# Kernel tuning notes

Measured on AMD Instinct MI355X. Metric: run time of the kernel, lower is better.

## Reference

```python
import jax, jax.numpy as jnp
import numpy as np

N_MBED = 384
HEAD_SIZE = 64

def setup_inputs() -> dict:
    key = jax.random.key(0)
    kx, kq, kk, kv = jax.random.split(key, 4)
    B, T = 128, 256
    x = jax.random.normal(kx, (B, T, N_MBED), dtype=jnp.float32)
    # torch nn.Linear(n_mbed, head_size, bias=False): y = x @ W^T, W:[head_size, n_mbed].
    # We store the transposed weight [n_mbed, head_size] so y = x @ W.
    s = 1.0 / np.sqrt(N_MBED)
    Wq = jax.random.uniform(kq, (N_MBED, HEAD_SIZE), jnp.float32, -s, s)
    Wk = jax.random.uniform(kk, (N_MBED, HEAD_SIZE), jnp.float32, -s, s)
    Wv = jax.random.uniform(kv, (N_MBED, HEAD_SIZE), jnp.float32, -s, s)
    return {"x": x, "Wq": Wq, "Wk": Wk, "Wv": Wv}

def reference(x, Wq, Wk, Wv):
    B, T, C = x.shape  # C = n_mbed = 384
    q = x @ Wq  # [B,T,H]
    k = x @ Wk
    v = x @ Wv
    # Faithful to source: wei = k @ q^T, scaled by C**-0.5 (C = n_mbed, not head_size)
    wei = jnp.einsum('bth,bsh->bts', k, q) * (C ** -0.5)  # [B,T,T]
    mask = jnp.tril(jnp.ones((T, T), dtype=bool))
    wei = jnp.where(mask, wei, -jnp.inf)
    wei = jax.nn.softmax(wei, axis=-1)
    # dropout omitted (eval mode / identity)
    out = jnp.einsum('bts,bsh->bth', wei, v)  # [B,T,H]
    return out
```

## Files before the change

### kernel.cpp

```cpp
#include <hip/hip_runtime.h>
#include <hip/hip_bf16.h>
#include <math.h>

constexpr int kB = 128;
constexpr int kT = 256;
constexpr int kC = 384;
constexpr int kH = 64;

using bf16x8 = __attribute__((ext_vector_type(8))) short;
using f32x4  = __attribute__((ext_vector_type(4))) float;

union BF8 { bf16x8 v; __hip_bfloat162 h[4]; };
union BF4 { short4 s; __hip_bfloat162 h[2]; };

__device__ inline bf16x8 cvt8(float4 a, float4 b) {
    BF8 u;
    u.h[0] = __float22bfloat162_rn(float2{a.x, a.y});
    u.h[1] = __float22bfloat162_rn(float2{a.z, a.w});
    u.h[2] = __float22bfloat162_rn(float2{b.x, b.y});
    u.h[3] = __float22bfloat162_rn(float2{b.z, b.w});
    return u.v;
}
__device__ inline short4 cvt4(float4 a) {
    BF4 u;
    u.h[0] = __float22bfloat162_rn(float2{a.x, a.y});
    u.h[1] = __float22bfloat162_rn(float2{a.z, a.w});
    return u.s;
}

__global__ void prep_kernel(const float* __restrict__ Wq,
                            const float* __restrict__ Wk,
                            const float* __restrict__ Wv,
                            __hip_bfloat16* __restrict__ Wt) {
    int idx = blockIdx.x * 256 + threadIdx.x;
    int n = idx / kC, c = idx % kC;
    int w = n >> 6, h = n & 63;
    const float* W = (w == 0) ? Wq : (w == 1) ? Wk : Wv;
    float val = W[c * kH + h];
    if (w == 1) val *= 0.051031036307982884f;
    Wt[idx] = __float2bfloat16(val);
}

__global__ __launch_bounds__(512, 4) void qkv_kernel(
    const float* __restrict__ x, const __hip_bfloat16* __restrict__ Wt,
    __hip_bfloat16* __restrict__ q, __hip_bfloat16* __restrict__ k,
    __hip_bfloat16* __restrict__ vT)
{
    __shared__ short As[2][64 * 72];
    __shared__ short Bs[2][192 * 72];

    const int tid  = threadIdx.x;
    const int wave = tid >> 6, lane = tid & 63;
    const int m16  = lane & 15, quad = lane >> 4;
    const int wm = wave & 1, wn = wave >> 1;
    const int m0 = blockIdx.x * 64;
    const short* wt = (const short*)Wt;

    const bool stageA = (tid < 256);
    const int am  = tid >> 2;
    const int ak0 = (tid & 3) * 16;
    const int bu  = tid - 256;

    float4 la[4]; bf16x8 lb[6];
    auto glod = [&](int k0) {
        if (stageA) {
#pragma unroll
            for (int i = 0; i < 4; ++i)
                la[i] = *(const float4*)(x + (size_t)(m0 + am) * kC + k0 + ak0 + 4 * i);
        } else {
#pragma unroll
            for (int i = 0; i < 6; ++i) {
                int c = bu + 256 * i;
                int n = c >> 3, kk = (c & 7) * 8;
                lb[i] = *(const bf16x8*)(wt + (size_t)n * kC + k0 + kk);
            }
        }
    };
    auto swr = [&](int d) {
        if (stageA) {
#pragma unroll
            for (int i = 0; i < 4; ++i)
                *(short4*)&As[d][am * 72 + ak0 + 4 * i] = cvt4(la[i]);
        } else {
#pragma unroll
            for (int i = 0; i < 6; ++i) {
                int c = bu + 256 * i;
                int n = c >> 3, kk = (c & 7) * 8;
                *(bf16x8*)&Bs[d][n * 72 + kk] = lb[i];
            }
        }
    };

    f32x4 acc[2][3];
#pragma unroll
    for (int mt = 0; mt < 2; ++mt)
#pragma unroll
        for (int j = 0; j < 3; ++j) acc[mt][j] = f32x4{0.f, 0.f, 0.f, 0.f};

    glod(0);
    swr(0);
    __syncthreads();

    for (int s = 0; s < 6; ++s) {
        const int d = s & 1;
        if (s < 5) glod((s + 1) * 64);

#pragma unroll
        for (int kf = 0; kf < 2; ++kf) {
            bf16x8 af[2], bfr[3];
#pragma unroll
            for (int mt = 0; mt < 2; ++mt)
                af[mt] = *(const bf16x8*)&As[d][(wm * 32 + mt * 16 + m16) * 72 + kf * 32 + quad * 8];
#pragma unroll
            for (int j = 0; j < 3; ++j)
                bfr[j] = *(const bf16x8*)&Bs[d][(wn * 48 + j * 16 + m16) * 72 + kf * 32 + quad * 8];
#pragma unroll
            for (int mt = 0; mt < 2; ++mt)
#pragma unroll
                for (int j = 0; j < 3; ++j)
                    acc[mt][j] = __builtin_amdgcn_mfma_f32_16x16x32_bf16(
                        af[mt], bfr[j], acc[mt][j], 0, 0, 0);
        }

        if (s < 5) swr(d ^ 1);
        __syncthreads();
    }

#pragma unroll
    for (int mt = 0; mt < 2; ++mt) {
#pragma unroll
        for (int j = 0; j < 3; ++j) {
            const int n = wn * 48 + j * 16 + m16;
            const int w = n >> 6, h = n & 63;
#pragma unroll
            for (int r = 0; r < 4; ++r) {
                const int m = m0 + wm * 32 + mt * 16 + quad * 4 + r;
                __hip_bfloat16 val = __float2bfloat16(acc[mt][j][r]);
                if (w == 0)      q[(size_t)m * kH + h] = val;
                else if (w == 1) k[(size_t)m * kH + h] = val;
                else             vT[((size_t)(m >> 8) * kH + h) * kT + (m & 255)] = val;
            }
        }
    }
}

__global__ __launch_bounds__(256) void attn_kernel(
    const __hip_bfloat16* __restrict__ qg, const __hip_bfloat16* __restrict__ kg,
    const __hip_bfloat16* __restrict__ vTg, float* __restrict__ out)
{
    __shared__ short Qs[2][64 * 72];
    __shared__ short Vs[2][64 * 72];
    __shared__ float Ps[4][16 * 68];

    const int b  = blockIdx.y;
    const int tq = blockIdx.x;
    const int tid  = threadIdx.x;
    const int wave = tid >> 6, lane = tid & 63;
    const int m16  = lane & 15, quad = lane >> 4;
    const int tband = tq * 64 + wave * 16;

    const short* qs = (const short*)qg + (size_t)b * kT * kH;
    const short* ks = (const short*)kg + (size_t)b * kT * kH;
    const short* vs = (const short*)vTg + (size_t)b * kH * kT;

    const bf16x8 ka0 = *(const bf16x8*)(ks + (size_t)(tband + m16) * kH + quad * 8);
    const bf16x8 ka1 = *(const bf16x8*)(ks + (size_t)(tband + m16) * kH + quad * 8 + 32);

    const int r0 = tid >> 3, sg = (tid & 7) * 8;

    bf16x8 lq0, lq1, lv0, lv1;
    auto glod = [&](int sc) {
        lq0 = *(const bf16x8*)(qs + (size_t)(sc + r0) * kH + sg);
        lq1 = *(const bf16x8*)(qs + (size_t)(sc + r0 + 32) * kH + sg);
        lv0 = *(const bf16x8*)(vs + (size_t)r0 * kT + sc + sg);
        lv1 = *(const bf16x8*)(vs + (size_t)(r0 + 32) * kT + sc + sg);
    };
    auto swr = [&](int d) {
        *(bf16x8*)&Qs[d][r0 * 72 + sg]        = lq0;
        *(bf16x8*)&Qs[d][(r0 + 32) * 72 + sg] = lq1;
        *(bf16x8*)&Vs[d][r0 * 72 + sg]        = lv0;
        *(bf16x8*)&Vs[d][(r0 + 32) * 72 + sg] = lv1;
    };

    f32x4 O[4];
    float m_[4], l_[4];
#pragma unroll
    for (int i = 0; i < 4; ++i) {
        O[i] = f32x4{0.f, 0.f, 0.f, 0.f};
        m_[i] = -INFINITY; l_[i] = 0.f;
    }
    float* Pw = &Ps[wave][0];

    glod(0);
    swr(0);
    __syncthreads();

    for (int i = 0; i <= tq; ++i) {
        const int d = i & 1;
        if (i < tq) glod((i + 1) * 64);

        const int jmax = (i == tq) ? wave : 3;

        f32x4 S[4];
        const f32x4 Z = f32x4{0.f, 0.f, 0.f, 0.f};
#pragma unroll
        for (int j = 0; j < 4; ++j) {
            if (j <= jmax) {
                bf16x8 qb0 = *(const bf16x8*)&Qs[d][(j * 16 + m16) * 72 + quad * 8];
                bf16x8 qb1 = *(const bf16x8*)&Qs[d][(j * 16 + m16) * 72 + 32 + quad * 8];
                S[j] = __builtin_amdgcn_mfma_f32_16x16x32_bf16(ka0, qb0, Z, 0, 0, 0);
                S[j] = __builtin_amdgcn_mfma_f32_16x16x32_bf16(ka1, qb1, S[j], 0, 0, 0);
            }
        }
        if (i == tq) {
#pragma unroll
            for (int r = 0; r < 4; ++r)
                if (m16 > quad * 4 + r) S[wave][r] = -INFINITY;
        }

        float P[4][4];
#pragma unroll
        for (int j = 0; j < 4; ++j)
#pragma unroll
            for (int r = 0; r < 4; ++r) P[j][r] = 0.f;
#pragma unroll
        for (int r = 0; r < 4; ++r) {
            float rm = -INFINITY;
#pragma unroll
            for (int j = 0; j < 4; ++j)
                if (j <= jmax) rm = fmaxf(rm, S[j][r]);
            rm = fmaxf(rm, __shfl_xor(rm, 1, 64));
            rm = fmaxf(rm, __shfl_xor(rm, 2, 64));
            rm = fmaxf(rm, __shfl_xor(rm, 4, 64));
            rm = fmaxf(rm, __shfl_xor(rm, 8, 64));
            const float mn = fmaxf(m_[r], rm);
            const float al = __expf(m_[r] - mn);
            m_[r] = mn;
            float rs = 0.f;
#pragma unroll
            for (int j = 0; j < 4; ++j) {
                if (j <= jmax) { P[j][r] = __expf(S[j][r] - mn); rs += P[j][r]; }
            }
            rs += __shfl_xor(rs, 1, 64);
            rs += __shfl_xor(rs, 2, 64);
            rs += __shfl_xor(rs, 4, 64);
            rs += __shfl_xor(rs, 8, 64);
            l_[r] = l_[r] * al + rs;
            O[0][r] *= al; O[1][r] *= al; O[2][r] *= al; O[3][r] *= al;
        }

#pragma unroll
        for (int j = 0; j < 4; ++j)
#pragma unroll
            for (int r = 0; r < 4; ++r)
                Pw[(quad * 4 + r) * 68 + j * 16 + m16] = P[j][r];
        const float* pr = Pw + m16 * 68 + quad * 8;
        bf16x8 pf0 = cvt8(*(const float4*)pr,        *(const float4*)(pr + 4));
        bf16x8 pf1 = cvt8(*(const float4*)(pr + 32), *(const float4*)(pr + 36));

#pragma unroll
        for (int ht = 0; ht < 4; ++ht) {
            bf16x8 vb0 = *(const bf16x8*)&Vs[d][(ht * 16 + m16) * 72 + quad * 8];
            bf16x8 vb1 = *(const bf16x8*)&Vs[d][(ht * 16 + m16) * 72 + 32 + quad * 8];
            O[ht] = __builtin_amdgcn_mfma_f32_16x16x32_bf16(pf0, vb0, O[ht], 0, 0, 0);
            O[ht] = __builtin_amdgcn_mfma_f32_16x16x32_bf16(pf1, vb1, O[ht], 0, 0, 0);
        }

        if (i < tq) swr(d ^ 1);
        __syncthreads();
    }

#pragma unroll
    for (int r = 0; r < 4; ++r) {
        const float inv = 1.f / l_[r];
        const size_t row = (size_t)(b * kT + tband + quad * 4 + r);
#pragma unroll
        for (int ht = 0; ht < 4; ++ht)
            out[row * kH + ht * 16 + m16] = O[ht][r] * inv;
    }
}

extern "C" void kernel_launch(void* const* d_in, const int* in_sizes, int n_in,
                              void* d_out, int out_size, void* d_ws, size_t ws_size,
                              hipStream_t stream) {
    const float* x  = (const float*)d_in[0];
    const float* Wq = (const float*)d_in[1];
    const float* Wk = (const float*)d_in[2];
    const float* Wv = (const float*)d_in[3];
    float* out = (float*)d_out;

    const size_t nqkv = (size_t)kB * kT * kH;
    __hip_bfloat16* q  = (__hip_bfloat16*)d_ws;
    __hip_bfloat16* k  = q + nqkv;
    __hip_bfloat16* vT = k + nqkv;
    __hip_bfloat16* Wt = vT + nqkv;

    prep_kernel<<<(192 * kC) / 256, 256, 0, stream>>>(Wq, Wk, Wv, Wt);
    qkv_kernel<<<(kB * kT) / 64, 512, 0, stream>>>(x, Wt, q, k, vT);
    attn_kernel<<<dim3(4, kB), 256, 0, stream>>>(q, k, vT, out);
}
```

Measured before the change: 117.4 us.

## Fuse QKV projection and causal attention into one per-batch-half kernel

Merges the QKV projection and attention kernels into one kernel. Each block handles one batch and one 128-row half of the queries, computes the needed Q/K/V^T rows directly into shared memory, then runs attention without global round-trips for q/k/vT. This removes the intermediate global traffic and a launch. In exchange the grid shrinks to 256 blocks of 512 threads, shared-memory use grows large, and the second half recomputes the projections of the first 128 rows.

```diff
diff --git a/kernel.cpp b/kernel.cpp
--- a/kernel.cpp
+++ b/kernel.cpp
@@ -26,6 +26,10 @@
     u.h[0] = __float22bfloat162_rn(float2{a.x, a.y});
     u.h[1] = __float22bfloat162_rn(float2{a.z, a.w});
     return u.s;
+}
+__device__ inline short bf1(float f) {
+    __hip_bfloat16 h = __float2bfloat16(f);
+    return *(short*)&h;
 }
 
 __global__ void prep_kernel(const float* __restrict__ Wq,
@@ -41,20 +45,28 @@
     Wt[idx] = __float2bfloat16(val);
 }
 
-__global__ __launch_bounds__(512, 4) void qkv_kernel(
+__global__ __launch_bounds__(512, 2) void fused_kernel(
     const float* __restrict__ x, const __hip_bfloat16* __restrict__ Wt,
-    __hip_bfloat16* __restrict__ q, __hip_bfloat16* __restrict__ k,
-    __hip_bfloat16* __restrict__ vT)
+    float* __restrict__ out)
 {
-    __shared__ short As[2][64 * 72];
-    __shared__ short Bs[2][192 * 72];
+    __shared__ short Qs[256 * 68];
+    __shared__ short VTs[64 * 260];
+    __shared__ short Ks[128 * 68];
+    __shared__ __attribute__((aligned(16))) char STG[73728];
+    short (*As)[64 * 72]  = (short (*)[64 * 72])STG;
+    short (*Bs)[192 * 72] = (short (*)[192 * 72])(STG + 18432);
+
+    const int b    = blockIdx.y;
+    const int half = (int)blockIdx.x ^ 1;
+    const int t0   = half * 128;
+    const int nmc  = (t0 + 128) >> 6;
 
     const int tid  = threadIdx.x;
     const int wave = tid >> 6, lane = tid & 63;
     const int m16  = lane & 15, quad = lane >> 4;
     const int wm = wave & 1, wn = wave >> 1;
-    const int m0 = blockIdx.x * 64;
     const short* wt = (const short*)Wt;
+    const float* xb = x + (size_t)b * kT * kC;
 
     const bool stageA = (tid < 256);
     const int am  = tid >> 2;
@@ -62,11 +74,11 @@
     const int bu  = tid - 256;
 
     float4 la[4]; bf16x8 lb[6];
-    auto glod = [&](int k0) {
+    auto glod = [&](int m0, int k0) {
         if (stageA) {
 #pragma unroll
             for (int i = 0; i < 4; ++i)
-                la[i] = *(const float4*)(x + (size_t)(m0 + am) * kC + k0 + ak0 + 4 * i);
+                la[i] = *(const float4*)(xb + (size_t)(m0 + am) * kC + k0 + ak0 + 4 * i);
         } else {
 #pragma unroll
             for (int i = 0; i < 6; ++i) {
@@ -91,96 +103,74 @@
         }
     };
 
-    f32x4 acc[2][3];
-#pragma unroll
-    for (int mt = 0; mt < 2; ++mt)
-#pragma unroll
-        for (int j = 0; j < 3; ++j) acc[mt][j] = f32x4{0.f, 0.f, 0.f, 0.f};
-
-    glod(0);
-    swr(0);
+    for (int mc = 0; mc < nmc; ++mc) {
+        const int m0 = mc * 64;
+
+        f32x4 acc[2][3];
+#pragma unroll
+        for (int mt = 0; mt < 2; ++mt)
+#pragma unroll
+            for (int j = 0; j < 3; ++j) acc[mt][j] = f32x4{0.f, 0.f, 0.f, 0.f};
+
+        glod(m0, 0);
+        swr(0);
+        __syncthreads();
+
+        for (int s = 0; s < 6; ++s) {
+            const int d = s & 1;
+            if (s < 5) glod(m0, (s + 1) * 64);
+#pragma unroll
+            for (int kf = 0; kf < 2; ++kf) {
+                bf16x8 af[2], bfr[3];
+#pragma unroll
+                for (int mt = 0; mt < 2; ++mt)
+                    af[mt] = *(const bf16x8*)&As[d][(wm * 32 + mt * 16 + m16) * 72 + kf * 32 + quad * 8];
+#pragma unroll
+                for (int j = 0; j < 3; ++j)
+                    bfr[j] = *(const bf16x8*)&Bs[d][(wn * 48 + j * 16 + m16) * 72 + kf * 32 + quad * 8];
+#pragma unroll
+                for (int mt = 0; mt < 2; ++mt)
+#pragma unroll
+                    for (int j = 0; j < 3; ++j)
+                        acc[mt][j] = __builtin_amdgcn_mfma_f32_16x16x32_bf16(
+                            af[mt], bfr[j], acc[mt][j], 0, 0, 0);
+            }
+            if (s < 5) swr(d ^ 1);
+            __syncthreads();
+        }
+
+#pragma unroll
+        for (int mt = 0; mt < 2; ++mt) {
+            const int mbase = m0 + wm * 32 + mt * 16 + quad * 4;
+#pragma unroll
+            for (int j = 0; j < 3; ++j) {
+                const int n = wn * 48 + j * 16 + m16;
+                const int w = n >> 6, h = n & 63;
+                if (w == 2) {
+                    float4 f = make_float4(acc[mt][j][0], acc[mt][j][1],
+                                           acc[mt][j][2], acc[mt][j][3]);
+                    *(short4*)&VTs[h * 260 + mbase] = cvt4(f);
+                } else if (w == 1) {
+                    if (m0 >= t0) {
+#pragma unroll
+                        for (int r = 0; r < 4; ++r)
+                            Ks[(mbase + r - t0) * 68 + h] = bf1(acc[mt][j][r]);
+                    }
+                } else {
+#pragma unroll
+                    for (int r = 0; r < 4; ++r)
+                        Qs[(mbase + r) * 68 + h] = bf1(acc[mt][j][r]);
+                }
+            }
+        }
+    }
     __syncthreads();
 
-    for (int s = 0; s < 6; ++s) {
-        const int d = s & 1;
-        if (s < 5) glod((s + 1) * 64);
-
-#pragma unroll
-        for (int kf = 0; kf < 2; ++kf) {
-            bf16x8 af[2], bfr[3];
-#pragma unroll
-            for (int mt = 0; mt < 2; ++mt)
-                af[mt] = *(const bf16x8*)&As[d][(wm * 32 + mt * 16 + m16) * 72 + kf * 32 + quad * 8];
-#pragma unroll
-            for (int j = 0; j < 3; ++j)
-                bfr[j] = *(const bf16x8*)&Bs[d][(wn * 48 + j * 16 + m16) * 72 + kf * 32 + quad * 8];
-#pragma unroll
-            for (int mt = 0; mt < 2; ++mt)
-#pragma unroll
-                for (int j = 0; j < 3; ++j)
-                    acc[mt][j] = __builtin_amdgcn_mfma_f32_16x16x32_bf16(
-                        af[mt], bfr[j], acc[mt][j], 0, 0, 0);
-        }
-
-        if (s < 5) swr(d ^ 1);
-        __syncthreads();
-    }
-
-#pragma unroll
-    for (int mt = 0; mt < 2; ++mt) {
-#pragma unroll
-        for (int j = 0; j < 3; ++j) {
-            const int n = wn * 48 + j * 16 + m16;
-            const int w = n >> 6, h = n & 63;
-#pragma unroll
-            for (int r = 0; r < 4; ++r) {
-                const int m = m0 + wm * 32 + mt * 16 + quad * 4 + r;
-                __hip_bfloat16 val = __float2bfloat16(acc[mt][j][r]);
-                if (w == 0)      q[(size_t)m * kH + h] = val;
-                else if (w == 1) k[(size_t)m * kH + h] = val;
-                else             vT[((size_t)(m >> 8) * kH + h) * kT + (m & 255)] = val;
-            }
-        }
-    }
-}
-
-__global__ __launch_bounds__(256) void attn_kernel(
-    const __hip_bfloat16* __restrict__ qg, const __hip_bfloat16* __restrict__ kg,
-    const __hip_bfloat16* __restrict__ vTg, float* __restrict__ out)
-{
-    __shared__ short Qs[2][64 * 72];
-    __shared__ short Vs[2][64 * 72];
-    __shared__ float Ps[4][16 * 68];
-
-    const int b  = blockIdx.y;
-    const int tq = blockIdx.x;
-    const int tid  = threadIdx.x;
-    const int wave = tid >> 6, lane = tid & 63;
-    const int m16  = lane & 15, quad = lane >> 4;
-    const int tband = tq * 64 + wave * 16;
-
-    const short* qs = (const short*)qg + (size_t)b * kT * kH;
-    const short* ks = (const short*)kg + (size_t)b * kT * kH;
-    const short* vs = (const short*)vTg + (size_t)b * kH * kT;
-
-    const bf16x8 ka0 = *(const bf16x8*)(ks + (size_t)(tband + m16) * kH + quad * 8);
-    const bf16x8 ka1 = *(const bf16x8*)(ks + (size_t)(tband + m16) * kH + quad * 8 + 32);
-
-    const int r0 = tid >> 3, sg = (tid & 7) * 8;
-
-    bf16x8 lq0, lq1, lv0, lv1;
-    auto glod = [&](int sc) {
-        lq0 = *(const bf16x8*)(qs + (size_t)(sc + r0) * kH + sg);
-        lq1 = *(const bf16x8*)(qs + (size_t)(sc + r0 + 32) * kH + sg);
-        lv0 = *(const bf16x8*)(vs + (size_t)r0 * kT + sc + sg);
-        lv1 = *(const bf16x8*)(vs + (size_t)(r0 + 32) * kT + sc + sg);
-    };
-    auto swr = [&](int d) {
-        *(bf16x8*)&Qs[d][r0 * 72 + sg]        = lq0;
-        *(bf16x8*)&Qs[d][(r0 + 32) * 72 + sg] = lq1;
-        *(bf16x8*)&Vs[d][r0 * 72 + sg]        = lv0;
-        *(bf16x8*)&Vs[d][(r0 + 32) * 72 + sg] = lv1;
-    };
+    const int wband = t0 + wave * 16;
+    float* Pw = (float*)STG + wave * 16 * 68;
+
+    const bf16x8 ka0 = *(const bf16x8*)&Ks[(wave * 16 + m16) * 68 + quad * 8];
+    const bf16x8 ka1 = *(const bf16x8*)&Ks[(wave * 16 + m16) * 68 + quad * 8 + 32];
 
     f32x4 O[4];
     float m_[4], l_[4];
@@ -189,33 +179,27 @@
         O[i] = f32x4{0.f, 0.f, 0.f, 0.f};
         m_[i] = -INFINITY; l_[i] = 0.f;
     }
-    float* Pw = &Ps[wave][0];
-
-    glod(0);
-    swr(0);
-    __syncthreads();
-
-    for (int i = 0; i <= tq; ++i) {
-        const int d = i & 1;
-        if (i < tq) glod((i + 1) * 64);
-
-        const int jmax = (i == tq) ? wave : 3;
+
+    const int ilast = wband >> 6;
+    for (int i = 0; i <= ilast; ++i) {
+        const bool diag = (i == ilast);
+        const int jmax = diag ? (wave & 3) : 3;
 
         f32x4 S[4];
         const f32x4 Z = f32x4{0.f, 0.f, 0.f, 0.f};
 #pragma unroll
         for (int j = 0; j < 4; ++j) {
             if (j <= jmax) {
-                bf16x8 qb0 = *(const bf16x8*)&Qs[d][(j * 16 + m16) * 72 + quad * 8];
-                bf16x8 qb1 = *(const bf16x8*)&Qs[d][(j * 16 + m16) * 72 + 32 + quad * 8];
+                bf16x8 qb0 = *(const bf16x8*)&Qs[(i * 64 + j * 16 + m16) * 68 + quad * 8];
+                bf16x8 qb1 = *(const bf16x8*)&Qs[(i * 64 + j * 16 + m16) * 68 + quad * 8 + 32];
                 S[j] = __builtin_amdgcn_mfma_f32_16x16x32_bf16(ka0, qb0, Z, 0, 0, 0);
                 S[j] = __builtin_amdgcn_mfma_f32_16x16x32_bf16(ka1, qb1, S[j], 0, 0, 0);
             }
         }
-        if (i == tq) {
+        if (diag) {
 #pragma unroll
             for (int r = 0; r < 4; ++r)
-                if (m16 > quad * 4 + r) S[wave][r] = -INFINITY;
+                if (m16 > quad * 4 + r) S[jmax][r] = -INFINITY;
         }
 
         float P[4][4];
@@ -260,20 +244,17 @@
 
 #pragma unroll
         for (int ht = 0; ht < 4; ++ht) {
-            bf16x8 vb0 = *(const bf16x8*)&Vs[d][(ht * 16 + m16) * 72 + quad * 8];
-            bf16x8 vb1 = *(const bf16x8*)&Vs[d][(ht * 16 + m16) * 72 + 32 + quad * 8];
+            bf16x8 vb0 = *(const bf16x8*)&VTs[(ht * 16 + m16) * 260 + i * 64 + quad * 8];
+            bf16x8 vb1 = *(const bf16x8*)&VTs[(ht * 16 + m16) * 260 + i * 64 + quad * 8 + 32];
             O[ht] = __builtin_amdgcn_mfma_f32_16x16x32_bf16(pf0, vb0, O[ht], 0, 0, 0);
             O[ht] = __builtin_amdgcn_mfma_f32_16x16x32_bf16(pf1, vb1, O[ht], 0, 0, 0);
         }
-
-        if (i < tq) swr(d ^ 1);
-        __syncthreads();
     }
 
 #pragma unroll
     for (int r = 0; r < 4; ++r) {
         const float inv = 1.f / l_[r];
-        const size_t row = (size_t)(b * kT + tband + quad * 4 + r);
+        const size_t row = (size_t)(b * kT + wband + quad * 4 + r);
 #pragma unroll
         for (int ht = 0; ht < 4; ++ht)
             out[row * kH + ht * 16 + m16] = O[ht][r] * inv;
@@ -289,13 +270,8 @@
     const float* Wv = (const float*)d_in[3];
     float* out = (float*)d_out;
 
-    const size_t nqkv = (size_t)kB * kT * kH;
-    __hip_bfloat16* q  = (__hip_bfloat16*)d_ws;
-    __hip_bfloat16* k  = q + nqkv;
-    __hip_bfloat16* vT = k + nqkv;
-    __hip_bfloat16* Wt = vT + nqkv;
+    __hip_bfloat16* Wt = (__hip_bfloat16*)d_ws;
 
     prep_kernel<<<(192 * kC) / 256, 256, 0, stream>>>(Wq, Wk, Wv, Wt);
-    qkv_kernel<<<(kB * kT) / 64, 512, 0, stream>>>(x, Wt, q, k, vT);
-    attn_kernel<<<dim3(4, kB), 256, 0, stream>>>(q, k, vT, out);
-}
+    fused_kernel<<<dim3(2, kB), 512, 0, stream>>>(x, Wt, out);
+}
```

Result: slower. 123.5 us (+5.1%).
